# Kernel tuning notes

Measured on AMD Instinct MI355X. Metric: run time of the kernel, lower is better.

## Reference

```python
import jax, jax.numpy as jnp
import numpy as np

B, T, C = 2, 2048, 2048
NH = 16          # n_head
G = 4            # group_size
NKV = NH // G    # kv heads
HD = C // NH     # head_dim = 128
BASE = 10000.0


def setup_inputs() -> dict:
    key = jax.random.key(0)
    ks = jax.random.split(key, 9)
    s = 0.02
    return {
        "x": jax.random.normal(ks[0], (B, T, C), jnp.float32),
        "wq_w": jax.random.normal(ks[1], (C, C), jnp.float32) * s,
        "wq_b": jax.random.normal(ks[2], (C,), jnp.float32) * s,
        "wk_w": jax.random.normal(ks[3], (C // G, C), jnp.float32) * s,
        "wk_b": jax.random.normal(ks[4], (C // G,), jnp.float32) * s,
        "wv_w": jax.random.normal(ks[5], (C // G, C), jnp.float32) * s,
        "wv_b": jax.random.normal(ks[6], (C // G,), jnp.float32) * s,
        "cp_w": jax.random.normal(ks[7], (C, C), jnp.float32) * s,
        "cp_b": jax.random.normal(ks[8], (C,), jnp.float32) * s,
    }


def _rope(x):
    # Faithful to source: RoPE is applied to [B, H, T, HD] but the module
    # reads seq_len = x.size(1) == H, so the rotation angle is indexed by the
    # HEAD axis and broadcast over sequence positions.
    b, h, t, d = x.shape
    half = d // 2
    theta = 1.0 / (BASE ** (jnp.arange(0, half, dtype=jnp.float32) * 2.0 / d))  # [half]
    ang = jnp.arange(h, dtype=jnp.float32)[:, None] * theta[None, :]            # [h, half]
    cos = jnp.cos(ang)[None, :, None, :]  # [1, h, 1, half]
    sin = jnp.sin(ang)[None, :, None, :]
    xs = x.reshape(b, h, t, half, 2)
    x0, x1 = xs[..., 0], xs[..., 1]
    out = jnp.stack([x0 * cos - x1 * sin, x1 * cos + x0 * sin], axis=-1)
    return out.reshape(b, h, t, d)


def reference(x, wq_w, wq_b, wk_w, wk_b, wv_w, wv_b, cp_w, cp_b):
    b, t, c = x.shape
    q = x @ wq_w.T + wq_b                                  # [B,T,C]
    k = x @ wk_w.T + wk_b                                  # [B,T,C//G]
    v = x @ wv_w.T + wv_b                                  # [B,T,C//G]
    q = q.reshape(b, t, NH, HD).transpose(0, 2, 1, 3)      # [B,NH,T,HD]
    k = k.reshape(b, t, NKV, HD).transpose(0, 2, 1, 3)     # [B,NKV,T,HD]
    v = v.reshape(b, t, NKV, HD).transpose(0, 2, 1, 3)
    q = _rope(q)
    k = _rope(k)
    # GQA expand: each kv head repeated G times consecutively
    k = jnp.repeat(k, G, axis=1)                           # [B,NH,T,HD]
    v = jnp.repeat(v, G, axis=1)
    att = jnp.einsum('bhqd,bhkd->bhqk', q, k) / (HD ** 0.5)
    mask = jnp.tril(jnp.ones((t, t), dtype=bool))
    att = jnp.where(mask[None, None], att, -jnp.inf)
    att = jax.nn.softmax(att, axis=-1)
    y = jnp.einsum('bhqk,bhkd->bhqd', att, v)
    y = y.transpose(0, 2, 1, 3).reshape(b, t, c)
    return y @ cp_w.T + cp_b
```

## Files before the change

kernel.cpp:

```cpp
#include <hip/hip_runtime.h>

typedef unsigned short u16;
typedef __bf16 bf16x8 __attribute__((ext_vector_type(8)));
typedef float f32x4 __attribute__((ext_vector_type(4)));
typedef float f32x16 __attribute__((ext_vector_type(16)));
typedef unsigned u32x4 __attribute__((ext_vector_type(4)));

#define T_   2048
#define C_   2048
#define HD_  128
#define NH_  16
#define NKV_ 4
#define M_   4096

typedef __attribute__((address_space(1))) const void* as1_cvp;
typedef __attribute__((address_space(3))) void* as3_vp;

__device__ __forceinline__ void gload16(const void* g, void* l) {
  __builtin_amdgcn_global_load_lds((as1_cvp)g, (as3_vp)l, 16, 0, 0);
}

__device__ __forceinline__ u16 f2bf(float f) {
  unsigned u = __builtin_bit_cast(unsigned, f);
  return (u16)((u + 0x7fffu + ((u >> 16) & 1u)) >> 16);
}

__device__ __forceinline__ float fexp2(float x) {
  float r;
  asm("v_exp_f32 %0, %1" : "=v"(r) : "v"(x));
  return r;
}

__device__ __forceinline__ unsigned cvtpk(float a, float b) {
  unsigned d;
  asm("v_cvt_pk_bf16_f32 %0, %1, %2" : "=v"(d) : "v"(a), "v"(b));
  return d;
}

__global__ void cvt_bf16(const float4* __restrict__ in, ushort4* __restrict__ out, int n4) {
  int i = blockIdx.x * blockDim.x + threadIdx.x;
  if (i >= n4) return;
  float4 v = in[i];
  ushort4 r;
  r.x = f2bf(v.x); r.y = f2bf(v.y); r.z = f2bf(v.z); r.w = f2bf(v.w);
  out[i] = r;
}

__global__ void copy_f32(const float* __restrict__ in, float* __restrict__ out, int n) {
  int i = blockIdx.x * blockDim.x + threadIdx.x;
  if (i < n) out[i] = in[i];
}

__global__ void rope_fold_w(const float* __restrict__ W, u16* __restrict__ out, int npair) {
  int idx = blockIdx.x * blockDim.x + threadIdx.x;
  int p  = idx >> 9;
  int c4 = (idx & 511) << 2;
  if (p >= npair) return;
  int h  = p >> 6;
  int ii = p & 63;
  float theta = __expf(-(float)ii * (9.210340371976184f / 64.0f));
  float s, c;
  __sincosf((float)h * theta, &s, &c);
  size_t r0 = (size_t)(2 * p) * 2048 + c4;
  size_t r1 = r0 + 2048;
  float4 a = *(const float4*)(W + r0);
  float4 b = *(const float4*)(W + r1);
  ushort4 o0, o1;
  o0.x = f2bf(a.x * c - b.x * s); o0.y = f2bf(a.y * c - b.y * s);
  o0.z = f2bf(a.z * c - b.z * s); o0.w = f2bf(a.w * c - b.w * s);
  o1.x = f2bf(b.x * c + a.x * s); o1.y = f2bf(b.y * c + a.y * s);
  o1.z = f2bf(b.z * c + a.z * s); o1.w = f2bf(b.w * c + a.w * s);
  *(ushort4*)(out + r0) = o0;
  *(ushort4*)(out + r1) = o1;
}

__global__ void rope_fold_b(const float* __restrict__ bin, float* __restrict__ bout, int npair) {
  int p = blockIdx.x * blockDim.x + threadIdx.x;
  if (p >= npair) return;
  int h = p >> 6, ii = p & 63;
  float theta = __expf(-(float)ii * (9.210340371976184f / 64.0f));
  float s, c;
  __sincosf((float)h * theta, &s, &c);
  float a = bin[2 * p], b = bin[2 * p + 1];
  bout[2 * p]     = a * c - b * s;
  bout[2 * p + 1] = b * c + a * s;
}

template<int BN, int MODE>
__global__ __launch_bounds__(512)
void gemm8(const u16* __restrict__ A, const u16* __restrict__ W,
           const float* __restrict__ bias, void* __restrict__ op0,
           void* __restrict__ op1, void* __restrict__ op2, const float qscale) {
  constexpr int NREP = BN / 64;
  constexpr int ASZ  = 256 * 64;
  constexpr int BSZ  = BN * 64;
  constexpr int BUF  = ASZ + BSZ;
  constexpr int NB   = BSZ / 4096;
  __shared__ __align__(16) u16 sm[2 * BUF];
  const int tid  = threadIdx.x;
  const int lane = tid & 63;
  const int wid  = tid >> 6;
  const int wr = wid >> 2, wc = wid & 3;
  const int m0 = blockIdx.y << 8;
  const int n0 = blockIdx.x * BN;
  const int K  = C_;
  const int fr = lane & 15, g = lane >> 4;

  const u16* srcA[4]; int dstA[4];
#pragma unroll
  for (int i = 0; i < 4; ++i) {
    const int idx = i * 512 + tid;
    const int row = idx >> 3, sch = (idx & 7) ^ (row & 7);
    srcA[i] = A + (size_t)(m0 + row) * K + sch * 8;
    dstA[i] = idx * 8;
  }
  const u16* srcB[NB]; int dstB[NB];
#pragma unroll
  for (int i = 0; i < NB; ++i) {
    const int idx = i * 512 + tid;
    const int row = idx >> 3, sch = (idx & 7) ^ (row & 7);
    srcB[i] = W + (size_t)(n0 + row) * K + sch * 8;
    dstB[i] = ASZ + idx * 8;
  }
  const int swz0 = ((g     ^ (fr & 7)) << 3);
  const int swz1 = (((4+g) ^ (fr & 7)) << 3);

  f32x4 acc[8][NREP] = {};

#pragma unroll
  for (int i = 0; i < 4; ++i) gload16(srcA[i], sm + dstA[i]);
#pragma unroll
  for (int i = 0; i < NB; ++i) gload16(srcB[i], sm + dstB[i]);
  __syncthreads();

#define LDA(MH, SWZ) {                                                   \
  _Pragma("unroll")                                                      \
  for (int mi = 0; mi < 4; ++mi) {                                       \
    const int row = wr * 128 + (MH) * 64 + mi * 16 + fr;                 \
    af[mi] = *(const bf16x8*)&sm[base + row * 64 + (SWZ)];               \
  } }
#define LDB(BF, SWZ) {                                                   \
  _Pragma("unroll")                                                      \
  for (int ni = 0; ni < NREP; ++ni) {                                    \
    const int row = wc * (BN / 4) + ni * 16 + fr;                        \
    BF[ni] = *(const bf16x8*)&sm[base + ASZ + row * 64 + (SWZ)];         \
  } }
#define MM(MH, BF) {                                                     \
  __builtin_amdgcn_s_setprio(1);                                         \
  _Pragma("unroll")                                                      \
  for (int mi = 0; mi < 4; ++mi)                                         \
    _Pragma("unroll")                                                    \
    for (int ni = 0; ni < NREP; ++ni)                                    \
      acc[(MH) * 4 + mi][ni] = __builtin_amdgcn_mfma_f32_16x16x32_bf16(  \
          af[mi], BF[ni], acc[(MH) * 4 + mi][ni], 0, 0, 0);              \
  __builtin_amdgcn_s_setprio(0); }

  for (int t = 0; t < 32; ++t) {
    const int base = (t & 1) * BUF;
    const int pbuf = ((t & 1) ^ 1) * BUF;
    bf16x8 af[4], bfa[NREP], bfb[NREP];
    if (t < 31) {
      const int ko = (t + 1) * 64;
#pragma unroll
      for (int i = 0; i < 4; ++i) gload16(srcA[i] + ko, sm + pbuf + dstA[i]);
      __builtin_amdgcn_sched_barrier(0);
    }
    LDA(0, swz0) LDB(bfa, swz0) MM(0, bfa)
    __builtin_amdgcn_s_barrier();
    if (t < 31) {
      const int ko = (t + 1) * 64;
#pragma unroll
      for (int i = 0; i < NB; ++i) gload16(srcB[i] + ko, sm + pbuf + dstB[i]);
      __builtin_amdgcn_sched_barrier(0);
    }
    LDA(1, swz0) MM(1, bfa)
    __builtin_amdgcn_s_barrier();
    LDB(bfb, swz1) LDA(0, swz1) MM(0, bfb)
    __builtin_amdgcn_s_barrier();
    LDA(1, swz1) MM(1, bfb)
    __syncthreads();
  }
#undef LDA
#undef LDB
#undef MM

#pragma unroll
  for (int mh = 0; mh < 2; ++mh)
#pragma unroll
    for (int mi = 0; mi < 4; ++mi) {
      const int rg0 = m0 + wr * 128 + mh * 64 + mi * 16 + ((lane >> 4) << 2);
#pragma unroll
      for (int ni = 0; ni < NREP; ++ni) {
        const int cg = n0 + wc * (BN / 4) + ni * 16 + fr;
        const float bb = bias[cg];
#pragma unroll
        for (int r = 0; r < 4; ++r) {
          float v = acc[mh * 4 + mi][ni][r] + bb;
          const int rg = rg0 + r;
          if (MODE == 1) {
            ((float*)op0)[(size_t)rg * C_ + cg] = v;
          } else {
            const int b = rg >> 11, t = rg & (T_ - 1);
            if (cg < 2048) {
              const int h = cg >> 7, d = cg & 127;
              ((u16*)op0)[((((size_t)b * NH_ + h) * T_ + t) << 7) + d] = f2bf(v * qscale);
            } else if (cg < 2560) {
              const int c2 = cg - 2048, h = c2 >> 7, d = c2 & 127;
              ((u16*)op1)[((((size_t)b * NKV_ + h) * T_ + t) << 7) + d] = f2bf(v);
            } else {
              const int c2 = cg - 2560, h = c2 >> 7, d = c2 & 127;
              ((u16*)op2)[(((size_t)b * NKV_ + h) * HD_ + d) * T_ + t] = f2bf(v);
            }
          }
        }
      }
    }
}

__device__ __forceinline__ void stage_kv(u16* dst, const u16* __restrict__ kg,
                                         const u16* __restrict__ vg, int lane, int w) {
#pragma unroll
  for (int r = 0; r < 4; ++r) {
    const int row = r * 16 + w * 4 + (lane >> 4);
    const int cg  = (lane & 15) ^ (row & 7);
    gload16(kg + (size_t)row * 128 + cg * 8, dst + row * 128 + (lane & 15) * 8);
  }
#pragma unroll
  for (int r = 0; r < 4; ++r) {
    const int row = r * 32 + w * 8 + (lane >> 3);
    const int cg  = (lane & 7) ^ (row & 7);
    gload16(vg + (size_t)row * T_ + cg * 8, dst + 8192 + row * 64 + (lane & 7) * 8);
  }
}

__global__ __launch_bounds__(256, 2)
void attn2(const u16* __restrict__ q, const u16* __restrict__ k,
           const u16* __restrict__ vt, u16* __restrict__ y) {
  __shared__ __align__(16) u16 sm[32768];
  const int tid  = threadIdx.x;
  const int lane = tid & 63;
  const int w    = tid >> 6;
  const int hi   = lane >> 5;
  const int l5   = lane & 31;
  const int h = blockIdx.y;
  const int b = blockIdx.z;
  const int qt = b ? (int)blockIdx.x : (15 - (int)blockIdx.x);
  const int q0  = qt << 7;
  const int q0w = q0 + w * 32;
  const int nkv = 2 * qt + 2;
  const size_t qbase = (((size_t)b * NH_ + h) * T_ + q0) * HD_;
  const size_t kbase = ((size_t)b * NKV_ + (h >> 2)) * (size_t)T_ * HD_;
  const size_t vbase = ((size_t)b * NKV_ + (h >> 2)) * (size_t)HD_ * T_;

#pragma unroll
  for (int r = 0; r < 8; ++r) {
    const int row = r * 16 + w * 4 + (lane >> 4);
    const int cg  = (lane & 15) ^ (row & 7);
    gload16(q + qbase + (size_t)row * 128 + cg * 8, sm + row * 128 + (lane & 15) * 8);
  }
  __syncthreads();
  bf16x8 qf[8];
  {
    const int row = w * 32 + l5;
#pragma unroll
    for (int kd = 0; kd < 8; ++kd)
      qf[kd] = *(const bf16x8*)&sm[row * 128 + ((((kd << 1) | hi) ^ (row & 7)) << 3)];
  }
  __syncthreads();
  stage_kv(sm, k + kbase, vt + vbase, lane, w);

  f32x16 o[4] = {};
  float m = -1e30f, l = 0.f;

  for (int kv = 0; kv < nkv; ++kv) {
    __syncthreads();
    const int buf = kv & 1;
    if (kv + 1 < nkv)
      stage_kv(sm + ((buf ^ 1) << 14),
               k + kbase + ((size_t)(kv + 1) << 6) * 128,
               vt + vbase + ((kv + 1) << 6), lane, w);

    if ((kv << 6) <= q0w + 31) {
      const u16* Ks = sm + (buf << 14);
      const u16* Vs = Ks + 8192;

      f32x16 st[2] = {};
      __builtin_amdgcn_s_setprio(1);
#pragma unroll
      for (int kt = 0; kt < 2; ++kt) {
        const int krow = kt * 32 + l5;
#pragma unroll
        for (int kd = 0; kd < 8; ++kd) {
          bf16x8 ka = *(const bf16x8*)&Ks[krow * 128 + ((((kd << 1) | hi) ^ (l5 & 7)) << 3)];
          st[kt] = __builtin_amdgcn_mfma_f32_32x32x16_bf16(ka, qf[kd], st[kt], 0, 0, 0);
        }
      }
      __builtin_amdgcn_s_setprio(0);

      if ((kv << 6) + 63 > q0w) {
        const int qg = q0w + l5;
#pragma unroll
        for (int kt = 0; kt < 2; ++kt)
#pragma unroll
          for (int r = 0; r < 16; ++r) {
            const int kg = (kv << 6) + kt * 32 + (r & 3) + ((r >> 2) << 3) + (hi << 2);
            if (kg > qg) st[kt][r] = -3.0e38f;
          }
      }

      float pmax = -3.0e38f;
#pragma unroll
      for (int kt = 0; kt < 2; ++kt)
#pragma unroll
        for (int r = 0; r < 16; ++r) pmax = fmaxf(pmax, st[kt][r]);
      pmax = fmaxf(pmax, __shfl_xor(pmax, 32));
      if (!__all(pmax - m <= 8.0f)) {
        const float mn = fmaxf(m, pmax);
        const float f = fexp2(m - mn);
        m = mn;
        l *= f;
#pragma unroll
        for (int r = 0; r < 16; ++r) {
          const float fr = __shfl(f, (r & 3) + ((r >> 2) << 3) + (hi << 2));
          o[0][r] *= fr; o[1][r] *= fr; o[2][r] *= fr; o[3][r] *= fr;
        }
      }

      float rs = 0.f;
#pragma unroll
      for (int kt = 0; kt < 2; ++kt) {
#pragma unroll
        for (int s = 0; s < 2; ++s) {
          float e0 = fexp2(st[kt][8 * s + 0] - m), e1 = fexp2(st[kt][8 * s + 1] - m);
          float e2 = fexp2(st[kt][8 * s + 2] - m), e3 = fexp2(st[kt][8 * s + 3] - m);
          float e4 = fexp2(st[kt][8 * s + 4] - m), e5 = fexp2(st[kt][8 * s + 5] - m);
          float e6 = fexp2(st[kt][8 * s + 6] - m), e7 = fexp2(st[kt][8 * s + 7] - m);
          rs += ((e0 + e1) + (e2 + e3)) + ((e4 + e5) + (e6 + e7));
          const unsigned wL0 = cvtpk(e0, e1), wL1 = cvtpk(e2, e3);
          const unsigned wH0 = cvtpk(e4, e5), wH1 = cvtpk(e6, e7);
          const unsigned s0 = hi ? wL0 : wH0, s1 = hi ? wL1 : wH1;
          const unsigned r0 = __shfl_xor(s0, 32), r1 = __shfl_xor(s1, 32);
          u32x4 fw;
          fw.x = hi ? r0 : wL0; fw.y = hi ? r1 : wL1;
          fw.z = hi ? wH0 : r0; fw.w = hi ? wH1 : r1;
          const bf16x8 pa = __builtin_bit_cast(bf16x8, fw);
          const int ch = (((kt * 2 + s) << 1) | hi) ^ (l5 & 7);
          __builtin_amdgcn_s_setprio(1);
#pragma unroll
          for (int ds = 0; ds < 4; ++ds) {
            const int vrow = ds * 32 + l5;
            bf16x8 vb = *(const bf16x8*)&Vs[vrow * 64 + (ch << 3)];
            o[ds] = __builtin_amdgcn_mfma_f32_32x32x16_bf16(pa, vb, o[ds], 0, 0, 0);
          }
          __builtin_amdgcn_s_setprio(0);
        }
      }
      rs += __shfl_xor(rs, 32);
      l += rs;
    }
  }

  const float linv = 1.0f / l;
#pragma unroll
  for (int r = 0; r < 16; ++r) {
    const int crow = (r & 3) + ((r >> 2) << 3) + (hi << 2);
    const float lf = __shfl(linv, crow);
    const int qg = q0w + crow;
    const size_t rowoff = (((size_t)(b << 11) + qg) << 11) + (h << 7) + l5;
#pragma unroll
    for (int ds = 0; ds < 4; ++ds)
      y[rowoff + ds * 32] = f2bf(o[ds][r] * lf);
  }
}

extern "C" void kernel_launch(void* const* d_in, const int* in_sizes, int n_in,
                              void* d_out, int out_size, void* d_ws, size_t ws_size,
                              hipStream_t stream) {
  (void)in_sizes; (void)n_in; (void)out_size; (void)ws_size;
  const float* x    = (const float*)d_in[0];
  const float* wq_w = (const float*)d_in[1];
  const float* wq_b = (const float*)d_in[2];
  const float* wk_w = (const float*)d_in[3];
  const float* wk_b = (const float*)d_in[4];
  const float* wv_w = (const float*)d_in[5];
  const float* wv_b = (const float*)d_in[6];
  const float* cp_w = (const float*)d_in[7];
  const float* cp_b = (const float*)d_in[8];

  char* ws = (char*)d_ws;
  u16* xb  = (u16*)ws;  ws += (size_t)M_ * C_ * 2;
  u16* wqr = (u16*)ws;  ws += (size_t)C_ * C_ * 2;
  u16* wkr = (u16*)ws;  ws += (size_t)512 * C_ * 2;
  u16* wvb = (u16*)ws;  ws += (size_t)512 * C_ * 2;
  u16* cpb = (u16*)ws;  ws += (size_t)C_ * C_ * 2;
  u16* qb  = (u16*)ws;  ws += (size_t)M_ * C_ * 2;
  u16* kb  = (u16*)ws;  ws += (size_t)M_ * 512 * 2;
  u16* vtb = (u16*)ws;  ws += (size_t)M_ * 512 * 2;
  float* bqkv = (float*)ws; ws += 3072 * 4;
  u16* yb = xb;

  cvt_bf16<<<8192, 256, 0, stream>>>((const float4*)x,    (ushort4*)xb,  2097152);
  cvt_bf16<<<1024, 256, 0, stream>>>((const float4*)wv_w, (ushort4*)wvb, 262144);
  cvt_bf16<<<4096, 256, 0, stream>>>((const float4*)cp_w, (ushort4*)cpb, 1048576);
  rope_fold_w<<<2048, 256, 0, stream>>>(wq_w, wqr, 1024);
  rope_fold_w<<<512,  256, 0, stream>>>(wk_w, wkr, 256);
  rope_fold_b<<<4, 256, 0, stream>>>(wq_b, bqkv, 1024);
  rope_fold_b<<<1, 256, 0, stream>>>(wk_b, bqkv + 2048, 256);
  copy_f32<<<2, 256, 0, stream>>>(wv_b, bqkv + 2560, 512);

  const float qscale = 0.08838834764831843f * 1.4426950408889634f;
  gemm8<192, 0><<<dim3(16, 16), 512, 0, stream>>>(xb, wqr, bqkv, qb, kb, vtb, qscale);

  attn2<<<dim3(16, 16, 2), 256, 0, stream>>>(qb, kb, vtb, yb);

  gemm8<128, 1><<<dim3(16, 16), 512, 0, stream>>>(yb, cpb, cp_b, (float*)d_out,
                                                  nullptr, nullptr, 1.0f);
}
```

Measured before the change: 193.0 us.

## Triple-buffer A tiles in GEMM and replace per-iteration syncthreads with partial vmcnt waits

The GEMM mainloop now keeps three LDS buffers for the A tile and two for the B tile, so A is prefetched two k-steps ahead and B one step ahead. The end-of-iteration __syncthreads is replaced by an s_waitcnt on a partial vmcnt plus an s_barrier, which lets outstanding global-to-LDS loads for the next stage stay in flight across the iteration boundary. This aims to hide more global load latency, at the cost of extra shared memory per block (which may lower occupancy) and hand-tuned waitcnt counts that depend on how many loads each thread issues.

Result: no change. 192.0 us (-0.5%).

```diff
diff --git a/kernel.cpp b/kernel.cpp
--- a/kernel.cpp
+++ b/kernel.cpp
@@ -94,9 +94,9 @@
   constexpr int NREP = BN / 64;
   constexpr int ASZ  = 256 * 64;
   constexpr int BSZ  = BN * 64;
-  constexpr int BUF  = ASZ + BSZ;
   constexpr int NB   = BSZ / 4096;
-  __shared__ __align__(16) u16 sm[2 * BUF];
+  constexpr int BB0  = 3 * ASZ;
+  __shared__ __align__(16) u16 sm[3 * ASZ + 2 * BSZ];
   const int tid  = threadIdx.x;
   const int lane = tid & 63;
   const int wid  = tid >> 6;
@@ -120,30 +120,40 @@
     const int idx = i * 512 + tid;
     const int row = idx >> 3, sch = (idx & 7) ^ (row & 7);
     srcB[i] = W + (size_t)(n0 + row) * K + sch * 8;
-    dstB[i] = ASZ + idx * 8;
+    dstB[i] = idx * 8;
   }
   const int swz0 = ((g     ^ (fr & 7)) << 3);
   const int swz1 = (((4+g) ^ (fr & 7)) << 3);
 
   f32x4 acc[8][NREP] = {};
 
-#pragma unroll
-  for (int i = 0; i < 4; ++i) gload16(srcA[i], sm + dstA[i]);
-#pragma unroll
-  for (int i = 0; i < NB; ++i) gload16(srcB[i], sm + dstB[i]);
-  __syncthreads();
+#define STAGE_A(buf, ko) {                                               \
+  _Pragma("unroll")                                                      \
+  for (int i = 0; i < 4; ++i)                                            \
+    gload16(srcA[i] + (ko), sm + (buf) * ASZ + dstA[i]); }
+#define STAGE_B(buf, ko) {                                               \
+  _Pragma("unroll")                                                      \
+  for (int i = 0; i < NB; ++i)                                           \
+    gload16(srcB[i] + (ko), sm + BB0 + (buf) * BSZ + dstB[i]); }
+
+  STAGE_A(0, 0)
+  STAGE_B(0, 0)
+  STAGE_A(1, 64)
+  asm volatile("s_waitcnt vmcnt(4)" ::: "memory");
+  __builtin_amdgcn_s_barrier();
+  __builtin_amdgcn_sched_barrier(0);
 
 #define LDA(MH, SWZ) {                                                   \
   _Pragma("unroll")                                                      \
   for (int mi = 0; mi < 4; ++mi) {                                       \
     const int row = wr * 128 + (MH) * 64 + mi * 16 + fr;                 \
-    af[mi] = *(const bf16x8*)&sm[base + row * 64 + (SWZ)];               \
+    af[mi] = *(const bf16x8*)&sm[ard + row * 64 + (SWZ)];                \
   } }
 #define LDB(BF, SWZ) {                                                   \
   _Pragma("unroll")                                                      \
   for (int ni = 0; ni < NREP; ++ni) {                                    \
     const int row = wc * (BN / 4) + ni * 16 + fr;                        \
-    BF[ni] = *(const bf16x8*)&sm[base + ASZ + row * 64 + (SWZ)];         \
+    BF[ni] = *(const bf16x8*)&sm[brd + row * 64 + (SWZ)];                \
   } }
 #define MM(MH, BF) {                                                     \
   __builtin_amdgcn_s_setprio(1);                                         \
@@ -155,22 +165,20 @@
           af[mi], BF[ni], acc[(MH) * 4 + mi][ni], 0, 0, 0);              \
   __builtin_amdgcn_s_setprio(0); }
 
+  int a0 = 0;
   for (int t = 0; t < 32; ++t) {
-    const int base = (t & 1) * BUF;
-    const int pbuf = ((t & 1) ^ 1) * BUF;
+    int a2 = a0 + 2; if (a2 >= 3) a2 -= 3;
+    const int ard = a0 * ASZ;
+    const int brd = BB0 + (t & 1) * BSZ;
     bf16x8 af[4], bfa[NREP], bfb[NREP];
     if (t < 31) {
-      const int ko = (t + 1) * 64;
-#pragma unroll
-      for (int i = 0; i < 4; ++i) gload16(srcA[i] + ko, sm + pbuf + dstA[i]);
+      STAGE_B((t & 1) ^ 1, (t + 1) * 64)
       __builtin_amdgcn_sched_barrier(0);
     }
     LDA(0, swz0) LDB(bfa, swz0) MM(0, bfa)
     __builtin_amdgcn_s_barrier();
-    if (t < 31) {
-      const int ko = (t + 1) * 64;
-#pragma unroll
-      for (int i = 0; i < NB; ++i) gload16(srcB[i] + ko, sm + pbuf + dstB[i]);
+    if (t < 30) {
+      STAGE_A(a2, (t + 2) * 64)
       __builtin_amdgcn_sched_barrier(0);
     }
     LDA(1, swz0) MM(1, bfa)
@@ -178,11 +186,19 @@
     LDB(bfb, swz1) LDA(0, swz1) MM(0, bfb)
     __builtin_amdgcn_s_barrier();
     LDA(1, swz1) MM(1, bfb)
-    __syncthreads();
+    if (t < 30)       asm volatile("s_waitcnt vmcnt(4)" ::: "memory");
+    else if (t == 30) asm volatile("s_waitcnt vmcnt(0)" ::: "memory");
+    if (t < 31) {
+      __builtin_amdgcn_s_barrier();
+      __builtin_amdgcn_sched_barrier(0);
+    }
+    a0 = a0 + 1; if (a0 == 3) a0 = 0;
   }
 #undef LDA
 #undef LDB
 #undef MM
+#undef STAGE_A
+#undef STAGE_B
 
 #pragma unroll
   for (int mh = 0; mh < 2; ++mh)
```

## Replace double-buffered GEMM with 4-slot K=32 pipeline and wider QKV tile

Applied to the files above, without the earlier changes.

The GEMM's two-buffer K=64 loop is replaced by a four-slot ring of K=32 stages. Loads run three stages ahead and are gated by explicit vmcnt waits rather than full syncthreads. The LDS swizzle changes to fit 32-element rows. The QKV projection now uses BN=256 over a 12x16 grid instead of 192 over 16x16, with launch bounds set for 2 blocks per CU. The aim is to hide global latency better and cut barrier cost, at the risk of more registers, more LDS, and fewer blocks for the QKV GEMM.

New measurement: 225.2 us. 16.7% more time.

```diff
diff --git a/kernel.cpp b/kernel.cpp
--- a/kernel.cpp
+++ b/kernel.cpp
@@ -87,16 +87,15 @@
 }
 
 template<int BN, int MODE>
-__global__ __launch_bounds__(512)
-void gemm8(const u16* __restrict__ A, const u16* __restrict__ W,
-           const float* __restrict__ bias, void* __restrict__ op0,
-           void* __restrict__ op1, void* __restrict__ op2, const float qscale) {
+__global__ __launch_bounds__(512, 2)
+void gemm_p4(const u16* __restrict__ A, const u16* __restrict__ W,
+             const float* __restrict__ bias, void* __restrict__ op0,
+             void* __restrict__ op1, void* __restrict__ op2, const float qscale) {
   constexpr int NREP = BN / 64;
-  constexpr int ASZ  = 256 * 64;
-  constexpr int BSZ  = BN * 64;
-  constexpr int BUF  = ASZ + BSZ;
-  constexpr int NB   = BSZ / 4096;
-  __shared__ __align__(16) u16 sm[2 * BUF];
+  constexpr int SLOT = 8192 + BN * 32;
+  constexpr int NB   = BN / 128;
+  constexpr int NL   = 2 + NB;
+  __shared__ __align__(16) u16 sm[4 * SLOT];
   const int tid  = threadIdx.x;
   const int lane = tid & 63;
   const int wid  = tid >> 6;
@@ -105,84 +104,89 @@
   const int n0 = blockIdx.x * BN;
   const int K  = C_;
   const int fr = lane & 15, g = lane >> 4;
-
-  const u16* srcA[4]; int dstA[4];
-#pragma unroll
-  for (int i = 0; i < 4; ++i) {
-    const int idx = i * 512 + tid;
-    const int row = idx >> 3, sch = (idx & 7) ^ (row & 7);
-    srcA[i] = A + (size_t)(m0 + row) * K + sch * 8;
-    dstA[i] = idx * 8;
+  const int swz = ((g ^ (fr >> 2)) & 3) << 3;
+
+  const u16* srcA[2]; int dstA[2];
+#pragma unroll
+  for (int i = 0; i < 2; ++i) {
+    const int j = i * 512 + tid;
+    const int row = j >> 2, l = (j & 3) ^ ((row >> 2) & 3);
+    srcA[i] = A + (size_t)(m0 + row) * K + l * 8;
+    dstA[i] = j * 8;
   }
   const u16* srcB[NB]; int dstB[NB];
 #pragma unroll
   for (int i = 0; i < NB; ++i) {
-    const int idx = i * 512 + tid;
-    const int row = idx >> 3, sch = (idx & 7) ^ (row & 7);
-    srcB[i] = W + (size_t)(n0 + row) * K + sch * 8;
-    dstB[i] = ASZ + idx * 8;
-  }
-  const int swz0 = ((g     ^ (fr & 7)) << 3);
-  const int swz1 = (((4+g) ^ (fr & 7)) << 3);
+    const int j = i * 512 + tid;
+    const int row = j >> 2, l = (j & 3) ^ ((row >> 2) & 3);
+    srcB[i] = W + (size_t)(n0 + row) * K + l * 8;
+    dstB[i] = 8192 + j * 8;
+  }
 
   f32x4 acc[8][NREP] = {};
 
-#pragma unroll
-  for (int i = 0; i < 4; ++i) gload16(srcA[i], sm + dstA[i]);
-#pragma unroll
-  for (int i = 0; i < NB; ++i) gload16(srcB[i], sm + dstB[i]);
-  __syncthreads();
-
-#define LDA(MH, SWZ) {                                                   \
-  _Pragma("unroll")                                                      \
-  for (int mi = 0; mi < 4; ++mi) {                                       \
-    const int row = wr * 128 + (MH) * 64 + mi * 16 + fr;                 \
-    af[mi] = *(const bf16x8*)&sm[base + row * 64 + (SWZ)];               \
-  } }
-#define LDB(BF, SWZ) {                                                   \
-  _Pragma("unroll")                                                      \
-  for (int ni = 0; ni < NREP; ++ni) {                                    \
-    const int row = wc * (BN / 4) + ni * 16 + fr;                        \
-    BF[ni] = *(const bf16x8*)&sm[base + ASZ + row * 64 + (SWZ)];         \
-  } }
-#define MM(MH, BF) {                                                     \
-  __builtin_amdgcn_s_setprio(1);                                         \
-  _Pragma("unroll")                                                      \
-  for (int mi = 0; mi < 4; ++mi)                                         \
-    _Pragma("unroll")                                                    \
-    for (int ni = 0; ni < NREP; ++ni)                                    \
-      acc[(MH) * 4 + mi][ni] = __builtin_amdgcn_mfma_f32_16x16x32_bf16(  \
-          af[mi], BF[ni], acc[(MH) * 4 + mi][ni], 0, 0, 0);              \
-  __builtin_amdgcn_s_setprio(0); }
-
-  for (int t = 0; t < 32; ++t) {
-    const int base = (t & 1) * BUF;
-    const int pbuf = ((t & 1) ^ 1) * BUF;
-    bf16x8 af[4], bfa[NREP], bfb[NREP];
-    if (t < 31) {
-      const int ko = (t + 1) * 64;
-#pragma unroll
-      for (int i = 0; i < 4; ++i) gload16(srcA[i] + ko, sm + pbuf + dstA[i]);
+#define STAGE(c) {                                                        \
+    const int sb_ = ((c) & 3) * SLOT;                                     \
+    const int ko_ = (c) * 32;                                             \
+    gload16(srcA[0] + ko_, sm + sb_ + dstA[0]);                           \
+    gload16(srcA[1] + ko_, sm + sb_ + dstA[1]);                           \
+    _Pragma("unroll")                                                     \
+    for (int i = 0; i < NB; ++i)                                          \
+      gload16(srcB[i] + ko_, sm + sb_ + dstB[i]);                         \
+  }
+#define LDB_ALL {                                                         \
+    _Pragma("unroll")                                                     \
+    for (int ni = 0; ni < NREP; ++ni) {                                   \
+      const int row = wc * (BN / 4) + ni * 16 + fr;                       \
+      bq[ni] = *(const bf16x8*)&sm[cb + 8192 + row * 32 + swz];           \
+    } }
+#define LDA_MH(MH) {                                                      \
+    _Pragma("unroll")                                                     \
+    for (int mi = 0; mi < 4; ++mi) {                                      \
+      const int row = wr * 128 + (MH) * 64 + mi * 16 + fr;                \
+      af[mi] = *(const bf16x8*)&sm[cb + row * 32 + swz];                  \
+    } }
+#define MM_MH(MH) {                                                       \
+    __builtin_amdgcn_s_setprio(1);                                        \
+    _Pragma("unroll")                                                     \
+    for (int mi = 0; mi < 4; ++mi)                                        \
+      _Pragma("unroll")                                                   \
+      for (int ni = 0; ni < NREP; ++ni)                                   \
+        acc[(MH) * 4 + mi][ni] = __builtin_amdgcn_mfma_f32_16x16x32_bf16( \
+            af[mi], bq[ni], acc[(MH) * 4 + mi][ni], 0, 0, 0);             \
+    __builtin_amdgcn_s_setprio(0); }
+
+  STAGE(0) STAGE(1) STAGE(2)
+
+  for (int c = 0; c < 64; ++c) {
+    const int cb = (c & 3) * SLOT;
+    if (c < 62) {
+      if constexpr (NL == 4) asm volatile("s_waitcnt vmcnt(8)" ::: "memory");
+      else                   asm volatile("s_waitcnt vmcnt(6)" ::: "memory");
+    } else if (c == 62) {
+      if constexpr (NL == 4) asm volatile("s_waitcnt vmcnt(4)" ::: "memory");
+      else                   asm volatile("s_waitcnt vmcnt(3)" ::: "memory");
+    } else {
+      asm volatile("s_waitcnt vmcnt(0)" ::: "memory");
+    }
+    __builtin_amdgcn_s_barrier();
+    __builtin_amdgcn_sched_barrier(0);
+    if (c < 61) {
+      STAGE(c + 3)
       __builtin_amdgcn_sched_barrier(0);
     }
-    LDA(0, swz0) LDB(bfa, swz0) MM(0, bfa)
+    bf16x8 af[4], bq[NREP];
+    LDB_ALL
+    LDA_MH(0)
+    MM_MH(0)
     __builtin_amdgcn_s_barrier();
-    if (t < 31) {
-      const int ko = (t + 1) * 64;
-#pragma unroll
-      for (int i = 0; i < NB; ++i) gload16(srcB[i] + ko, sm + pbuf + dstB[i]);
-      __builtin_amdgcn_sched_barrier(0);
-    }
-    LDA(1, swz0) MM(1, bfa)
-    __builtin_amdgcn_s_barrier();
-    LDB(bfb, swz1) LDA(0, swz1) MM(0, bfb)
-    __builtin_amdgcn_s_barrier();
-    LDA(1, swz1) MM(1, bfb)
-    __syncthreads();
-  }
-#undef LDA
-#undef LDB
-#undef MM
+    LDA_MH(1)
+    MM_MH(1)
+  }
+#undef STAGE
+#undef LDB_ALL
+#undef LDA_MH
+#undef MM_MH
 
 #pragma unroll
   for (int mh = 0; mh < 2; ++mh)
@@ -409,10 +413,10 @@
   copy_f32<<<2, 256, 0, stream>>>(wv_b, bqkv + 2560, 512);
 
   const float qscale = 0.08838834764831843f * 1.4426950408889634f;
-  gemm8<192, 0><<<dim3(16, 16), 512, 0, stream>>>(xb, wqr, bqkv, qb, kb, vtb, qscale);
+  gemm_p4<256, 0><<<dim3(12, 16), 512, 0, stream>>>(xb, wqr, bqkv, qb, kb, vtb, qscale);
 
   attn2<<<dim3(16, 16, 2), 256, 0, stream>>>(qb, kb, vtb, yb);
 
-  gemm8<128, 1><<<dim3(16, 16), 512, 0, stream>>>(yb, cpb, cp_b, (float*)d_out,
-                                                  nullptr, nullptr, 1.0f);
-}
+  gemm_p4<128, 1><<<dim3(16, 16), 512, 0, stream>>>(yb, cpb, cp_b, (float*)d_out,
+                                                    nullptr, nullptr, 1.0f);
+}
```

## Restructure GEMM with triple-buffered A tiles and 4x2 warp layout

Applied to the files above, without the earlier changes.

Replaces the double-buffered GEMM with a version that triple-buffers A tiles and double-buffers B tiles. Loads are issued two k-steps ahead for A, and explicit vmcnt/lgkmcnt waits replace the full __syncthreads per iteration. The warp grid changes from 2x4 to 4x2, so each warp computes a 64-row by BN/2-column tile, which shifts the balance of A and B fragment reuse. The intent is to hide global-to-LDS latency better and reduce barrier stalls, at the cost of more LDS use and fragile hand-tuned wait counts.

Measured after the change: 191.2 us. Within noise of the previous version (-0.9%).

```diff
diff --git a/kernel.cpp b/kernel.cpp
--- a/kernel.cpp
+++ b/kernel.cpp
@@ -88,133 +88,138 @@
 
 template<int BN, int MODE>
 __global__ __launch_bounds__(512)
-void gemm8(const u16* __restrict__ A, const u16* __restrict__ W,
-           const float* __restrict__ bias, void* __restrict__ op0,
-           void* __restrict__ op1, void* __restrict__ op2, const float qscale) {
-  constexpr int NREP = BN / 64;
-  constexpr int ASZ  = 256 * 64;
-  constexpr int BSZ  = BN * 64;
-  constexpr int BUF  = ASZ + BSZ;
-  constexpr int NB   = BSZ / 4096;
-  __shared__ __align__(16) u16 sm[2 * BUF];
+void gemm10(const u16* __restrict__ A, const u16* __restrict__ W,
+            const float* __restrict__ bias, void* __restrict__ op0,
+            void* __restrict__ op1, void* __restrict__ op2, const float qscale) {
+  constexpr int NREP = BN / 32;
+  constexpr int ABUF = 16384;
+  constexpr int BBUF = BN * 64;
+  constexpr int NBL  = BN / 64;
+  __shared__ __align__(16) u16 sm[3 * ABUF + 2 * BBUF];
   const int tid  = threadIdx.x;
   const int lane = tid & 63;
   const int wid  = tid >> 6;
-  const int wr = wid >> 2, wc = wid & 3;
+  const int wr = wid >> 1, wc = wid & 1;
   const int m0 = blockIdx.y << 8;
   const int n0 = blockIdx.x * BN;
   const int K  = C_;
   const int fr = lane & 15, g = lane >> 4;
-
-  const u16* srcA[4]; int dstA[4];
-#pragma unroll
-  for (int i = 0; i < 4; ++i) {
-    const int idx = i * 512 + tid;
-    const int row = idx >> 3, sch = (idx & 7) ^ (row & 7);
-    srcA[i] = A + (size_t)(m0 + row) * K + sch * 8;
-    dstA[i] = idx * 8;
-  }
-  const u16* srcB[NB]; int dstB[NB];
-#pragma unroll
-  for (int i = 0; i < NB; ++i) {
-    const int idx = i * 512 + tid;
-    const int row = idx >> 3, sch = (idx & 7) ^ (row & 7);
-    srcB[i] = W + (size_t)(n0 + row) * K + sch * 8;
-    dstB[i] = ASZ + idx * 8;
-  }
-  const int swz0 = ((g     ^ (fr & 7)) << 3);
-  const int swz1 = (((4+g) ^ (fr & 7)) << 3);
-
-  f32x4 acc[8][NREP] = {};
-
-#pragma unroll
-  for (int i = 0; i < 4; ++i) gload16(srcA[i], sm + dstA[i]);
-#pragma unroll
-  for (int i = 0; i < NB; ++i) gload16(srcB[i], sm + dstB[i]);
-  __syncthreads();
-
-#define LDA(MH, SWZ) {                                                   \
-  _Pragma("unroll")                                                      \
-  for (int mi = 0; mi < 4; ++mi) {                                       \
-    const int row = wr * 128 + (MH) * 64 + mi * 16 + fr;                 \
-    af[mi] = *(const bf16x8*)&sm[base + row * 64 + (SWZ)];               \
-  } }
-#define LDB(BF, SWZ) {                                                   \
-  _Pragma("unroll")                                                      \
-  for (int ni = 0; ni < NREP; ++ni) {                                    \
-    const int row = wc * (BN / 4) + ni * 16 + fr;                        \
-    BF[ni] = *(const bf16x8*)&sm[base + ASZ + row * 64 + (SWZ)];         \
-  } }
-#define MM(MH, BF) {                                                     \
-  __builtin_amdgcn_s_setprio(1);                                         \
-  _Pragma("unroll")                                                      \
-  for (int mi = 0; mi < 4; ++mi)                                         \
-    _Pragma("unroll")                                                    \
-    for (int ni = 0; ni < NREP; ++ni)                                    \
-      acc[(MH) * 4 + mi][ni] = __builtin_amdgcn_mfma_f32_16x16x32_bf16(  \
-          af[mi], BF[ni], acc[(MH) * 4 + mi][ni], 0, 0, 0);              \
+  const int rs0 = ((g ^ (fr & 7)) << 3);
+  const int rs1 = (((4 + g) ^ (fr & 7)) << 3);
+
+  size_t sofA[4]; int sdstA[4];
+#pragma unroll
+  for (int l = 0; l < 4; ++l) {
+    const int j = l * 512 + tid, rl = j >> 3, sl = j & 7;
+    sofA[l] = (size_t)rl * K + ((sl ^ (rl & 7)) << 3);
+    sdstA[l] = j * 8;
+  }
+  size_t sofB[NBL]; int sdstB[NBL];
+#pragma unroll
+  for (int l = 0; l < NBL; ++l) {
+    const int j = l * 512 + tid, rl = j >> 3, sl = j & 7;
+    sofB[l] = (size_t)rl * K + ((sl ^ (rl & 7)) << 3);
+    sdstB[l] = j * 8;
+  }
+  const u16* Ab = A + (size_t)m0 * K;
+  const u16* Bb = W + (size_t)n0 * K;
+
+  f32x4 acc[4][NREP] = {};
+
+#define SA(l, ks, buf) gload16(Ab + (size_t)(ks) * 64 + sofA[l], sm + (buf) * ABUF + sdstA[l]);
+#define SB(l, ks, buf) gload16(Bb + (size_t)(ks) * 64 + sofB[l], sm + 3 * ABUF + (buf) * BBUF + sdstB[l]);
+#define LDA(RS) { _Pragma("unroll")                                       \
+  for (int mi = 0; mi < 4; ++mi) {                                        \
+    const int row = wr * 64 + mi * 16 + fr;                               \
+    af[mi] = *(const bf16x8*)&sm[ab + row * 64 + (RS)]; } }
+#define LDB(RS) { _Pragma("unroll")                                       \
+  for (int ni = 0; ni < NREP; ++ni) {                                     \
+    const int row = wc * (BN / 2) + ni * 16 + fr;                         \
+    bq[ni] = *(const bf16x8*)&sm[3 * ABUF + bb + row * 64 + (RS)]; } }
+#define MMQ { __builtin_amdgcn_s_setprio(1); _Pragma("unroll")            \
+  for (int mi = 0; mi < 4; ++mi) _Pragma("unroll")                        \
+    for (int ni = 0; ni < NREP; ++ni)                                     \
+      acc[mi][ni] = __builtin_amdgcn_mfma_f32_16x16x32_bf16(              \
+          af[mi], bq[ni], acc[mi][ni], 0, 0, 0);                          \
   __builtin_amdgcn_s_setprio(0); }
-
-  for (int t = 0; t < 32; ++t) {
-    const int base = (t & 1) * BUF;
-    const int pbuf = ((t & 1) ^ 1) * BUF;
-    bf16x8 af[4], bfa[NREP], bfb[NREP];
-    if (t < 31) {
-      const int ko = (t + 1) * 64;
-#pragma unroll
-      for (int i = 0; i < 4; ++i) gload16(srcA[i] + ko, sm + pbuf + dstA[i]);
-      __builtin_amdgcn_sched_barrier(0);
+#define LGKM0 { asm volatile("s_waitcnt lgkmcnt(0)" ::: "memory");        \
+                __builtin_amdgcn_sched_barrier(0); }
+
+#pragma unroll
+  for (int l = 0; l < NBL; ++l) SB(l, 0, 0)
+#pragma unroll
+  for (int l = 0; l < 4; ++l) SA(l, 0, 0)
+#pragma unroll
+  for (int l = 0; l < 4; ++l) SA(l, 1, 1)
+  asm volatile("s_waitcnt vmcnt(4)" ::: "memory");
+  __builtin_amdgcn_s_barrier();
+
+  int a0 = 0, a2 = 2;
+  for (int s = 0; s < 32; ++s) {
+    const int ab = a0 * ABUF;
+    const int bb = (s & 1) * BBUF;
+    const int b1 = (s & 1) ^ 1;
+    bf16x8 af[4], bq[NREP];
+    LDB(rs0) LDA(rs0)
+    if (s < 31) {
+#pragma unroll
+      for (int l = 0; l < NBL; ++l) SB(l, s + 1, b1)
     }
-    LDA(0, swz0) LDB(bfa, swz0) MM(0, bfa)
     __builtin_amdgcn_s_barrier();
-    if (t < 31) {
-      const int ko = (t + 1) * 64;
-#pragma unroll
-      for (int i = 0; i < NB; ++i) gload16(srcB[i] + ko, sm + pbuf + dstB[i]);
-      __builtin_amdgcn_sched_barrier(0);
+    LGKM0
+    MMQ
+    __builtin_amdgcn_s_barrier();
+    LDB(rs1) LDA(rs1)
+    if (s < 30) {
+#pragma unroll
+      for (int l = 0; l < 4; ++l) SA(l, s + 2, a2)
+      asm volatile("s_waitcnt vmcnt(4)" ::: "memory");
+    } else if (s == 30) {
+      asm volatile("s_waitcnt vmcnt(0)" ::: "memory");
     }
-    LDA(1, swz0) MM(1, bfa)
     __builtin_amdgcn_s_barrier();
-    LDB(bfb, swz1) LDA(0, swz1) MM(0, bfb)
+    LGKM0
+    MMQ
     __builtin_amdgcn_s_barrier();
-    LDA(1, swz1) MM(1, bfb)
-    __syncthreads();
-  }
+    a0 = (a0 == 2) ? 0 : a0 + 1;
+    a2 = (a2 == 2) ? 0 : a2 + 1;
+  }
+#undef SA
+#undef SB
 #undef LDA
 #undef LDB
-#undef MM
-
-#pragma unroll
-  for (int mh = 0; mh < 2; ++mh)
-#pragma unroll
-    for (int mi = 0; mi < 4; ++mi) {
-      const int rg0 = m0 + wr * 128 + mh * 64 + mi * 16 + ((lane >> 4) << 2);
-#pragma unroll
-      for (int ni = 0; ni < NREP; ++ni) {
-        const int cg = n0 + wc * (BN / 4) + ni * 16 + fr;
-        const float bb = bias[cg];
-#pragma unroll
-        for (int r = 0; r < 4; ++r) {
-          float v = acc[mh * 4 + mi][ni][r] + bb;
-          const int rg = rg0 + r;
-          if (MODE == 1) {
-            ((float*)op0)[(size_t)rg * C_ + cg] = v;
+#undef MMQ
+#undef LGKM0
+
+#pragma unroll
+  for (int mi = 0; mi < 4; ++mi) {
+    const int rg0 = m0 + wr * 64 + mi * 16 + ((lane >> 4) << 2);
+#pragma unroll
+    for (int ni = 0; ni < NREP; ++ni) {
+      const int cg = n0 + wc * (BN / 2) + ni * 16 + fr;
+      const float bb2 = bias[cg];
+#pragma unroll
+      for (int r = 0; r < 4; ++r) {
+        float v = acc[mi][ni][r] + bb2;
+        const int rg = rg0 + r;
+        if (MODE == 1) {
+          ((float*)op0)[(size_t)rg * C_ + cg] = v;
+        } else {
+          const int b = rg >> 11, t = rg & (T_ - 1);
+          if (cg < 2048) {
+            const int h = cg >> 7, d = cg & 127;
+            ((u16*)op0)[((((size_t)b * NH_ + h) * T_ + t) << 7) + d] = f2bf(v * qscale);
+          } else if (cg < 2560) {
+            const int c2 = cg - 2048, h = c2 >> 7, d = c2 & 127;
+            ((u16*)op1)[((((size_t)b * NKV_ + h) * T_ + t) << 7) + d] = f2bf(v);
           } else {
-            const int b = rg >> 11, t = rg & (T_ - 1);
-            if (cg < 2048) {
-              const int h = cg >> 7, d = cg & 127;
-              ((u16*)op0)[((((size_t)b * NH_ + h) * T_ + t) << 7) + d] = f2bf(v * qscale);
-            } else if (cg < 2560) {
-              const int c2 = cg - 2048, h = c2 >> 7, d = c2 & 127;
-              ((u16*)op1)[((((size_t)b * NKV_ + h) * T_ + t) << 7) + d] = f2bf(v);
-            } else {
-              const int c2 = cg - 2560, h = c2 >> 7, d = c2 & 127;
-              ((u16*)op2)[(((size_t)b * NKV_ + h) * HD_ + d) * T_ + t] = f2bf(v);
-            }
+            const int c2 = cg - 2560, h = c2 >> 7, d = c2 & 127;
+            ((u16*)op2)[(((size_t)b * NKV_ + h) * HD_ + d) * T_ + t] = f2bf(v);
           }
         }
       }
     }
+  }
 }
 
 __device__ __forceinline__ void stage_kv(u16* dst, const u16* __restrict__ kg,
@@ -409,10 +414,10 @@
   copy_f32<<<2, 256, 0, stream>>>(wv_b, bqkv + 2560, 512);
 
   const float qscale = 0.08838834764831843f * 1.4426950408889634f;
-  gemm8<192, 0><<<dim3(16, 16), 512, 0, stream>>>(xb, wqr, bqkv, qb, kb, vtb, qscale);
+  gemm10<192, 0><<<dim3(16, 16), 512, 0, stream>>>(xb, wqr, bqkv, qb, kb, vtb, qscale);
 
   attn2<<<dim3(16, 16, 2), 256, 0, stream>>>(qb, kb, vtb, yb);
 
-  gemm8<128, 1><<<dim3(16, 16), 512, 0, stream>>>(yb, cpb, cp_b, (float*)d_out,
-                                                  nullptr, nullptr, 1.0f);
-}
+  gemm10<128, 1><<<dim3(16, 16), 512, 0, stream>>>(yb, cpb, cp_b, (float*)d_out,
+                                                   nullptr, nullptr, 1.0f);
+}
```
